# Optimization experiments

Measured on AMD Instinct MI355X. Metric: run time of the kernel, lower is better.

Reference implementation:

```python
import jax, jax.numpy as jnp
import numpy as np

B, W, H, I, L = 64, 4096, 128, 128, 2


def setup_inputs() -> dict:
    key = jax.random.key(0)
    ks = jax.random.split(key, 16)
    f = lambda k, s: jax.random.normal(k, s, dtype=jnp.float32) * 0.05
    return dict(
        input=f(ks[0], (B, 1, I)),
        h0=f(ks[1], (L, B, H)),
        c0=f(ks[2], (L, B, H)),
        encoder_output=f(ks[3], (B, W, H)),
        att_W=f(ks[4], (1, 2 * H)), att_b=f(ks[5], (1,)),
        inp_W=f(ks[6], (I, H + I)), inp_b=f(ks[7], (I,)),
        W_ih0=f(ks[8], (4 * H, I)), W_hh0=f(ks[9], (4 * H, H)),
        b_ih0=f(ks[10], (4 * H,)), b_hh0=f(ks[11], (4 * H,)),
        W_ih1=f(ks[12], (4 * H, H)), W_hh1=f(ks[13], (4 * H, H)),
        b_ih1=f(ks[14], (4 * H,)), b_hh1=f(ks[15], (4 * H,)),
    )


def _lstm_cell(x, h, c, W_ih, W_hh, b_ih, b_hh):
    # PyTorch gate order: i, f, g, o
    gates = x @ W_ih.T + h @ W_hh.T + b_ih + b_hh
    i, f, g, o = jnp.split(gates, 4, axis=-1)
    c_new = jax.nn.sigmoid(f) * c + jax.nn.sigmoid(i) * jnp.tanh(g)
    h_new = jax.nn.sigmoid(o) * jnp.tanh(c_new)
    return h_new, c_new


def reference(input, h0, c0, encoder_output, att_W, att_b, inp_W, inp_b,
              W_ih0, W_hh0, b_ih0, b_hh0, W_ih1, W_hh1, b_ih1, b_hh1):
    att_state = h0[-1] * c0[-1]                       # (B, H)
    # att_line over concat(enc_word, att_state): split the (1, 2H) weight.
    wa_enc, wa_st = att_W[0, :H], att_W[0, H:]
    scores = encoder_output @ wa_enc + (att_state @ wa_st + att_b[0])[:, None]  # (B, W)
    # Faithful to original: a leading zeros column is prepended, then
    # softmax is taken over [:, 0:-1] -> keeps the zero column, drops the
    # LAST word's score.
    zero_col = jnp.zeros((scores.shape[0], 1), scores.dtype)
    full = jnp.concatenate([zero_col, scores], axis=1)  # (B, W+1)
    weight = jax.nn.softmax(full[:, :-1], axis=1)        # (B, W)
    x = jnp.einsum('bw,bwh->bh', weight, encoder_output)  # (B, H)
    xin = jnp.concatenate([x, input[:, 0, :]], axis=1) @ inp_W.T + inp_b  # (B, I)
    # 2-layer LSTM, single time step (eval mode -> inter-layer dropout off)
    h1, c1 = _lstm_cell(xin, h0[0], c0[0], W_ih0, W_hh0, b_ih0, b_hh0)
    h2, c2 = _lstm_cell(h1, h0[1], c0[1], W_ih1, W_hh1, b_ih1, b_hh1)
    output = h2[:, None, :]                              # (B, 1, H)
    return output, jnp.stack([h1, h2]), jnp.stack([c1, c2])
```

## Files before the change

kernel.cpp:

```cpp
#include <hip/hip_runtime.h>
#include <hip/hip_bf16.h>

#define BB 64
#define WW 4096
#define HH 128

typedef unsigned short u16;
typedef unsigned int u32;

__device__ inline float bf2f(u16 u) {
    return __uint_as_float(((u32)u) << 16);
}
__device__ inline u16 f2bf(float f) {
    __hip_bfloat16 h = __float2bfloat16(f);
    return *reinterpret_cast<u16*>(&h);
}
__device__ inline void bf8_unpack(const uint4 r, float* o) {
    o[0] = __uint_as_float(r.x << 16);
    o[1] = __uint_as_float(r.x & 0xffff0000u);
    o[2] = __uint_as_float(r.y << 16);
    o[3] = __uint_as_float(r.y & 0xffff0000u);
    o[4] = __uint_as_float(r.z << 16);
    o[5] = __uint_as_float(r.z & 0xffff0000u);
    o[6] = __uint_as_float(r.w << 16);
    o[7] = __uint_as_float(r.w & 0xffff0000u);
}
__device__ inline float sigmoidf(float x) { return 1.0f / (1.0f + expf(-x)); }

template<bool FP32>
__device__ inline float ld1(const void* p, size_t i) {
    if (FP32) return ((const float*)p)[i];
    return bf2f(((const u16*)p)[i]);
}
template<bool FP32>
__device__ inline void ld8(const void* p, size_t g, float* o) {
    if (FP32) {
        float4 a = ((const float4*)p)[2 * g];
        float4 b = ((const float4*)p)[2 * g + 1];
        o[0] = a.x; o[1] = a.y; o[2] = a.z; o[3] = a.w;
        o[4] = b.x; o[5] = b.y; o[6] = b.z; o[7] = b.w;
    } else {
        uint4 r = ((const uint4*)p)[g];
        bf8_unpack(r, o);
    }
}
template<bool FP32>
__device__ inline void st1(void* p, size_t i, float v) {
    if (FP32) ((float*)p)[i] = v;
    else      ((u16*)p)[i] = f2bf(v);
}

__global__ void sniff_kernel(const u32* __restrict__ encw, float* __restrict__ flag) {
    __shared__ int red[256];
    const int t = threadIdx.x;
    u32 w = encw[(size_t)t * 997];
    float v = bf2f((u16)(w & 0xffffu));
    red[t] = (fabsf(v) <= 4.0f) ? 1 : 0;
    __syncthreads();
    for (int s = 128; s > 0; s >>= 1) {
        if (t < s) red[t] += red[t + s];
        __syncthreads();
    }
    if (t == 0) flag[0] = (red[0] >= 240) ? 1.0f : 0.0f;
}

template<bool FP32>
__global__ void scores_kernel(const void* __restrict__ enc,
                              const void* __restrict__ h0,
                              const void* __restrict__ c0,
                              const void* __restrict__ attW,
                              const void* __restrict__ attb,
                              const float* __restrict__ flag,
                              float* __restrict__ scores) {
    if ((flag[0] < 0.5f) != FP32) return;
    __shared__ float s_red[128];
    __shared__ float s_wa[128];
    __shared__ float s_bias;
    const int t = threadIdx.x;
    const int b = blockIdx.x >> 4;

    if (t < 128) {
        s_wa[t] = ld1<FP32>(attW, t);
        float hv = ld1<FP32>(h0, BB * HH + b * HH + t);
        float cv = ld1<FP32>(c0, BB * HH + b * HH + t);
        float ws = ld1<FP32>(attW, HH + t);
        s_red[t] = hv * cv * ws;
    }
    __syncthreads();
    for (int s = 64; s > 0; s >>= 1) {
        if (t < s) s_red[t] += s_red[t + s];
        __syncthreads();
    }
    if (t == 0) s_bias = s_red[0] + ld1<FP32>(attb, 0);
    __syncthreads();
    const float bias = s_bias;

    const int seg = t & 15;
    const int rg  = t >> 4;
    float wseg[8];
#pragma unroll
    for (int j = 0; j < 8; j++) wseg[j] = s_wa[seg * 8 + j];

    const size_t rowbase = (size_t)blockIdx.x * 256;
#pragma unroll 4
    for (int pass = 0; pass < 16; pass++) {
        const size_t row = rowbase + pass * 16 + rg;
        float v[8];
        ld8<FP32>(enc, row * 16 + seg, v);
        float d = 0.f;
#pragma unroll
        for (int j = 0; j < 8; j++) d += v[j] * wseg[j];
        d += __shfl_xor(d, 8, 16);
        d += __shfl_xor(d, 4, 16);
        d += __shfl_xor(d, 2, 16);
        d += __shfl_xor(d, 1, 16);
        if (seg == 0) scores[row] = d + bias;
    }
}

__global__ void softmax_kernel(const float* __restrict__ scores,
                               float* __restrict__ weight) {
    __shared__ float red[256];
    const int b = blockIdx.x;
    const int t = threadIdx.x;

    float lmax = -1e30f;
    for (int j = t; j < WW; j += 256) {
        float v = (j == 0) ? 0.f : scores[b * WW + j - 1];
        lmax = fmaxf(lmax, v);
    }
    red[t] = lmax;
    __syncthreads();
    for (int s = 128; s > 0; s >>= 1) {
        if (t < s) red[t] = fmaxf(red[t], red[t + s]);
        __syncthreads();
    }
    const float m = red[0];
    __syncthreads();

    float lsum = 0.f;
    for (int j = t; j < WW; j += 256) {
        float v = (j == 0) ? 0.f : scores[b * WW + j - 1];
        lsum += expf(v - m);
    }
    red[t] = lsum;
    __syncthreads();
    for (int s = 128; s > 0; s >>= 1) {
        if (t < s) red[t] += red[t + s];
        __syncthreads();
    }
    const float inv = 1.0f / red[0];
    __syncthreads();

    for (int j = t; j < WW; j += 256) {
        float v = (j == 0) ? 0.f : scores[b * WW + j - 1];
        weight[b * WW + j] = expf(v - m) * inv;
    }
}

__global__ void zero_x(float* __restrict__ x) {
    x[blockIdx.x * 1024 + threadIdx.x] = 0.f;
}

template<bool FP32>
__global__ void wsum_kernel(const void* __restrict__ enc,
                            const float* __restrict__ weight,
                            const float* __restrict__ flag,
                            float* __restrict__ x) {
    if ((flag[0] < 0.5f) != FP32) return;
    __shared__ float red[16 * 128];
    const int b = blockIdx.x >> 4;
    const int chunk = blockIdx.x & 15;
    const int t = threadIdx.x;
    const int seg = t & 15;
    const int wsub = t >> 4;

    float acc[8];
#pragma unroll
    for (int j = 0; j < 8; j++) acc[j] = 0.f;

    const int wbase = chunk * 256;
#pragma unroll 4
    for (int i = 0; i < 16; i++) {
        const int w = wbase + wsub + 16 * i;
        const float wt = weight[b * WW + w];
        float v[8];
        ld8<FP32>(enc, ((size_t)(b * WW + w)) * 16 + seg, v);
#pragma unroll
        for (int j = 0; j < 8; j++) acc[j] += wt * v[j];
    }
#pragma unroll
    for (int j = 0; j < 8; j++) red[wsub * 128 + seg * 8 + j] = acc[j];
    __syncthreads();
    if (t < 128) {
        float s = 0.f;
#pragma unroll
        for (int w2 = 0; w2 < 16; w2++) s += red[w2 * 128 + t];
        atomicAdd(&x[b * HH + t], s);
    }
}

template<bool FP32>
__global__ void xin_kernel(const float* __restrict__ x,
                           const void* __restrict__ input,
                           const void* __restrict__ inpW,
                           const void* __restrict__ inpb,
                           const float* __restrict__ flag,
                           float* __restrict__ xin) {
    if ((flag[0] < 0.5f) != FP32) return;
    __shared__ float xc[256];
    const int b = blockIdx.x;
    const int t = threadIdx.x;
    xc[t] = x[b * HH + t];
    xc[128 + t] = ld1<FP32>(input, b * HH + t);
    __syncthreads();
    float acc = ld1<FP32>(inpb, t);
#pragma unroll
    for (int k = 0; k < 256; k += 8) {
        float v[8];
        ld8<FP32>(inpW, ((size_t)t * 256 + k) >> 3, v);
#pragma unroll
        for (int j = 0; j < 8; j++) acc += xc[k + j] * v[j];
    }
    xin[b * HH + t] = acc;
}

template<bool FP32>
__global__ void lstm_kernel(const float* __restrict__ xv_in,
                            const void* __restrict__ hprev,
                            const void* __restrict__ cprev,
                            const void* __restrict__ W_ih,
                            const void* __restrict__ W_hh,
                            const void* __restrict__ b_ih,
                            const void* __restrict__ b_hh,
                            const float* __restrict__ flag,
                            float* __restrict__ hF_out,
                            void* __restrict__ h_out,
                            void* __restrict__ h_out2,
                            void* __restrict__ c_out) {
    if ((flag[0] < 0.5f) != FP32) return;
    __shared__ float xv[128];
    __shared__ float hv[128];
    __shared__ float gates[512];
    const int b = blockIdx.x;
    const int t = threadIdx.x;

    if (t < 128) {
        xv[t] = xv_in[b * HH + t];
        hv[t] = ld1<FP32>(hprev, b * HH + t);
    }
    __syncthreads();

    float acc = ld1<FP32>(b_ih, t) + ld1<FP32>(b_hh, t);
#pragma unroll
    for (int k = 0; k < 128; k += 8) {
        float v1[8], v2[8];
        ld8<FP32>(W_ih, ((size_t)t * 128 + k) >> 3, v1);
        ld8<FP32>(W_hh, ((size_t)t * 128 + k) >> 3, v2);
#pragma unroll
        for (int j = 0; j < 8; j++) acc += xv[k + j] * v1[j] + hv[k + j] * v2[j];
    }
    gates[t] = acc;
    __syncthreads();

    if (t < 128) {
        float ig = sigmoidf(gates[t]);
        float fg = sigmoidf(gates[128 + t]);
        float gg = tanhf(gates[256 + t]);
        float og = sigmoidf(gates[384 + t]);
        float cn = fg * ld1<FP32>(cprev, b * HH + t) + ig * gg;
        float hn = og * tanhf(cn);
        if (hF_out) hF_out[b * HH + t] = hn;
        st1<FP32>(h_out, b * HH + t, hn);
        if (h_out2) st1<FP32>(h_out2, b * HH + t, hn);
        st1<FP32>(c_out, b * HH + t, cn);
    }
}

extern "C" void kernel_launch(void* const* d_in, const int* in_sizes, int n_in,
                              void* d_out, int out_size, void* d_ws, size_t ws_size,
                              hipStream_t stream) {
    const void* input = d_in[0];
    const void* h0    = d_in[1];
    const void* c0    = d_in[2];
    const void* enc   = d_in[3];
    const void* attW  = d_in[4];
    const void* attb  = d_in[5];
    const void* inpW  = d_in[6];
    const void* inpb  = d_in[7];
    const void* Wih0  = d_in[8];
    const void* Whh0  = d_in[9];
    const void* bih0  = d_in[10];
    const void* bhh0  = d_in[11];
    const void* Wih1  = d_in[12];
    const void* Whh1  = d_in[13];
    const void* bih1  = d_in[14];
    const void* bhh1  = d_in[15];

    char* outc = (char*)d_out;

    float* wsf    = (float*)d_ws;
    float* scores = wsf;
    float* weight = wsf + (size_t)BB * WW;
    float* x      = weight + (size_t)BB * WW;
    float* xin    = x + BB * HH;
    float* h1f    = xin + BB * HH;
    float* flag   = h1f + BB * HH;

    sniff_kernel<<<1, 256, 0, stream>>>((const u32*)enc, flag);

    scores_kernel<false><<<BB * WW / 256, 256, 0, stream>>>(enc, h0, c0, attW, attb, flag, scores);
    scores_kernel<true ><<<BB * WW / 256, 256, 0, stream>>>(enc, h0, c0, attW, attb, flag, scores);
    softmax_kernel<<<BB, 256, 0, stream>>>(scores, weight);
    zero_x<<<8, 1024, 0, stream>>>(x);
    wsum_kernel<false><<<BB * 16, 256, 0, stream>>>(enc, weight, flag, x);
    wsum_kernel<true ><<<BB * 16, 256, 0, stream>>>(enc, weight, flag, x);
    xin_kernel<false><<<BB, 128, 0, stream>>>(x, input, inpW, inpb, flag, xin);
    xin_kernel<true ><<<BB, 128, 0, stream>>>(x, input, inpW, inpb, flag, xin);

    void* o_h1_b = outc + 8192 * 2;  void* o_h1_f = outc + 8192 * 4;
    void* o_h2_b = outc + 16384 * 2; void* o_h2_f = outc + 16384 * 4;
    void* o_c1_b = outc + 24576 * 2; void* o_c1_f = outc + 24576 * 4;
    void* o_c2_b = outc + 32768 * 2; void* o_c2_f = outc + 32768 * 4;

    lstm_kernel<false><<<BB, 512, 0, stream>>>(xin, h0, c0, Wih0, Whh0, bih0, bhh0, flag,
                                               h1f, o_h1_b, (void*)nullptr, o_c1_b);
    lstm_kernel<true ><<<BB, 512, 0, stream>>>(xin, h0, c0, Wih0, Whh0, bih0, bhh0, flag,
                                               h1f, o_h1_f, (void*)nullptr, o_c1_f);

    const char* h0l1_b = (const char*)h0 + BB * HH * 2;
    const char* c0l1_b = (const char*)c0 + BB * HH * 2;
    const char* h0l1_f = (const char*)h0 + BB * HH * 4;
    const char* c0l1_f = (const char*)c0 + BB * HH * 4;

    lstm_kernel<false><<<BB, 512, 0, stream>>>(h1f, h0l1_b, c0l1_b, Wih1, Whh1, bih1, bhh1, flag,
                                               (float*)nullptr, o_h2_b, d_out, o_c2_b);
    lstm_kernel<true ><<<BB, 512, 0, stream>>>(h1f, h0l1_f, c0l1_f, Wih1, Whh1, bih1, bhh1, flag,
                                               (float*)nullptr, o_h2_f, d_out, o_c2_f);
}
```

Baseline: 319.1 us.

## Fuse scores, softmax and weighted sum into one flash-style attention kernel

Replaces the sniff/scores/softmax/wsum/xin/lstm kernel chain with two kernels. The first computes chunk-local scores, an online softmax max and sum, and the weighted encoder sum in one pass, writing per-chunk partials. A tail kernel merges the partials and runs the input projection plus both LSTM layers. This drops the bf16/fp32 dual-launch path and the scores/weight round trips through global memory. The encoder is still read twice per chunk, the second time shifted by one row, though the second read may hit cache.

Result: faster. 285.6 us (-10.5%).

```diff
diff --git a/kernel.cpp b/kernel.cpp
--- a/kernel.cpp
+++ b/kernel.cpp
@@ -1,97 +1,43 @@
 #include <hip/hip_runtime.h>
-#include <hip/hip_bf16.h>
 
 #define BB 64
 #define WW 4096
 #define HH 128
-
-typedef unsigned short u16;
-typedef unsigned int u32;
-
-__device__ inline float bf2f(u16 u) {
-    return __uint_as_float(((u32)u) << 16);
-}
-__device__ inline u16 f2bf(float f) {
-    __hip_bfloat16 h = __float2bfloat16(f);
-    return *reinterpret_cast<u16*>(&h);
-}
-__device__ inline void bf8_unpack(const uint4 r, float* o) {
-    o[0] = __uint_as_float(r.x << 16);
-    o[1] = __uint_as_float(r.x & 0xffff0000u);
-    o[2] = __uint_as_float(r.y << 16);
-    o[3] = __uint_as_float(r.y & 0xffff0000u);
-    o[4] = __uint_as_float(r.z << 16);
-    o[5] = __uint_as_float(r.z & 0xffff0000u);
-    o[6] = __uint_as_float(r.w << 16);
-    o[7] = __uint_as_float(r.w & 0xffff0000u);
-}
+#define NCHUNK 32
+#define CROWS 128
+#define PSTRIDE 132
+
 __device__ inline float sigmoidf(float x) { return 1.0f / (1.0f + expf(-x)); }
 
-template<bool FP32>
-__device__ inline float ld1(const void* p, size_t i) {
-    if (FP32) return ((const float*)p)[i];
-    return bf2f(((const u16*)p)[i]);
-}
-template<bool FP32>
-__device__ inline void ld8(const void* p, size_t g, float* o) {
-    if (FP32) {
-        float4 a = ((const float4*)p)[2 * g];
-        float4 b = ((const float4*)p)[2 * g + 1];
-        o[0] = a.x; o[1] = a.y; o[2] = a.z; o[3] = a.w;
-        o[4] = b.x; o[5] = b.y; o[6] = b.z; o[7] = b.w;
-    } else {
-        uint4 r = ((const uint4*)p)[g];
-        bf8_unpack(r, o);
-    }
-}
-template<bool FP32>
-__device__ inline void st1(void* p, size_t i, float v) {
-    if (FP32) ((float*)p)[i] = v;
-    else      ((u16*)p)[i] = f2bf(v);
-}
-
-__global__ void sniff_kernel(const u32* __restrict__ encw, float* __restrict__ flag) {
-    __shared__ int red[256];
+__global__ void fused_attention(const float* __restrict__ enc,
+                                const float* __restrict__ h0,
+                                const float* __restrict__ c0,
+                                const float* __restrict__ attW,
+                                const float* __restrict__ attb,
+                                float* __restrict__ partials) {
+    __shared__ float s_wa[128];
+    __shared__ float s_red[128];
+    __shared__ float s_sc[CROWS];
+    __shared__ float racc[16 * 128];
+    __shared__ float s_bias, s_m, s_l;
+
     const int t = threadIdx.x;
-    u32 w = encw[(size_t)t * 997];
-    float v = bf2f((u16)(w & 0xffffu));
-    red[t] = (fabsf(v) <= 4.0f) ? 1 : 0;
-    __syncthreads();
-    for (int s = 128; s > 0; s >>= 1) {
-        if (t < s) red[t] += red[t + s];
-        __syncthreads();
-    }
-    if (t == 0) flag[0] = (red[0] >= 240) ? 1.0f : 0.0f;
-}
-
-template<bool FP32>
-__global__ void scores_kernel(const void* __restrict__ enc,
-                              const void* __restrict__ h0,
-                              const void* __restrict__ c0,
-                              const void* __restrict__ attW,
-                              const void* __restrict__ attb,
-                              const float* __restrict__ flag,
-                              float* __restrict__ scores) {
-    if ((flag[0] < 0.5f) != FP32) return;
-    __shared__ float s_red[128];
-    __shared__ float s_wa[128];
-    __shared__ float s_bias;
-    const int t = threadIdx.x;
-    const int b = blockIdx.x >> 4;
-
-    if (t < 128) {
-        s_wa[t] = ld1<FP32>(attW, t);
-        float hv = ld1<FP32>(h0, BB * HH + b * HH + t);
-        float cv = ld1<FP32>(c0, BB * HH + b * HH + t);
-        float ws = ld1<FP32>(attW, HH + t);
-        s_red[t] = hv * cv * ws;
+    const int b = blockIdx.x >> 5;
+    const int chunk = blockIdx.x & 31;
+    const int w0 = chunk * CROWS;
+
+    if (t < 128) {
+        s_wa[t] = attW[t];
+        float hv = h0[BB * HH + b * HH + t];
+        float cv = c0[BB * HH + b * HH + t];
+        s_red[t] = hv * cv * attW[HH + t];
     }
     __syncthreads();
     for (int s = 64; s > 0; s >>= 1) {
         if (t < s) s_red[t] += s_red[t + s];
         __syncthreads();
     }
-    if (t == 0) s_bias = s_red[0] + ld1<FP32>(attb, 0);
+    if (t == 0) s_bias = s_red[0] + attb[0];
     __syncthreads();
     const float bias = s_bias;
 
@@ -101,240 +47,223 @@
 #pragma unroll
     for (int j = 0; j < 8; j++) wseg[j] = s_wa[seg * 8 + j];
 
-    const size_t rowbase = (size_t)blockIdx.x * 256;
-#pragma unroll 4
-    for (int pass = 0; pass < 16; pass++) {
-        const size_t row = rowbase + pass * 16 + rg;
-        float v[8];
-        ld8<FP32>(enc, row * 16 + seg, v);
-        float d = 0.f;
-#pragma unroll
-        for (int j = 0; j < 8; j++) d += v[j] * wseg[j];
+#pragma unroll
+    for (int pass = 0; pass < 8; pass++) {
+        const int r = pass * 16 + rg;
+        const size_t w = (size_t)w0 + r;
+        const float4* p = (const float4*)(enc + ((size_t)b * WW + w) * HH + seg * 8);
+        float4 a = p[0], c = p[1];
+        float d = a.x * wseg[0] + a.y * wseg[1] + a.z * wseg[2] + a.w * wseg[3]
+                + c.x * wseg[4] + c.y * wseg[5] + c.z * wseg[6] + c.w * wseg[7];
         d += __shfl_xor(d, 8, 16);
         d += __shfl_xor(d, 4, 16);
         d += __shfl_xor(d, 2, 16);
         d += __shfl_xor(d, 1, 16);
-        if (seg == 0) scores[row] = d + bias;
-    }
+        if (seg == 0) s_sc[r] = (w == WW - 1) ? -1e30f : (d + bias);
+    }
+    __syncthreads();
+
+    if (t < 64) s_red[t] = fmaxf(s_sc[t], s_sc[t + 64]);
+    __syncthreads();
+    for (int s = 32; s > 0; s >>= 1) {
+        if (t < s) s_red[t] = fmaxf(s_red[t], s_red[t + s]);
+        __syncthreads();
+    }
+    if (t == 0) s_m = s_red[0];
+    __syncthreads();
+    const float m = s_m;
+
+    if (t < 128) s_sc[t] = expf(s_sc[t] - m);
+    __syncthreads();
+    if (t < 64) s_red[t] = s_sc[t] + s_sc[t + 64];
+    __syncthreads();
+    for (int s = 32; s > 0; s >>= 1) {
+        if (t < s) s_red[t] += s_red[t + s];
+        __syncthreads();
+    }
+    if (t == 0) s_l = s_red[0];
+
+    const int wsub = t >> 4;
+    float acc8[8];
+#pragma unroll
+    for (int j = 0; j < 8; j++) acc8[j] = 0.f;
+#pragma unroll
+    for (int pass = 0; pass < 8; pass++) {
+        const int r = pass * 16 + wsub;
+        const size_t w = (size_t)w0 + r;
+        if (w + 1 < WW) {
+            const float pw = s_sc[r];
+            const float4* p = (const float4*)(enc + ((size_t)b * WW + w + 1) * HH + seg * 8);
+            float4 a = p[0], c = p[1];
+            acc8[0] += pw * a.x; acc8[1] += pw * a.y;
+            acc8[2] += pw * a.z; acc8[3] += pw * a.w;
+            acc8[4] += pw * c.x; acc8[5] += pw * c.y;
+            acc8[6] += pw * c.z; acc8[7] += pw * c.w;
+        }
+    }
+#pragma unroll
+    for (int j = 0; j < 8; j++) racc[wsub * 128 + seg * 8 + j] = acc8[j];
+    __syncthreads();
+
+    float* out = partials + (size_t)(b * NCHUNK + chunk) * PSTRIDE;
+    if (t < 128) {
+        float s = 0.f;
+#pragma unroll
+        for (int w2 = 0; w2 < 16; w2++) s += racc[w2 * 128 + t];
+        out[t] = s;
+    }
+    if (t == 128) out[128] = m;
+    if (t == 129) out[129] = s_l;
 }
 
-__global__ void softmax_kernel(const float* __restrict__ scores,
-                               float* __restrict__ weight) {
-    __shared__ float red[256];
+__global__ void tail_kernel(const float* __restrict__ partials,
+                            const float* __restrict__ enc,
+                            const float* __restrict__ input,
+                            const float* __restrict__ inpW,
+                            const float* __restrict__ inpb,
+                            const float* __restrict__ Wih0,
+                            const float* __restrict__ Whh0,
+                            const float* __restrict__ bih0,
+                            const float* __restrict__ bhh0,
+                            const float* __restrict__ Wih1,
+                            const float* __restrict__ Whh1,
+                            const float* __restrict__ bih1,
+                            const float* __restrict__ bhh1,
+                            const float* __restrict__ h0,
+                            const float* __restrict__ c0,
+                            float* __restrict__ out) {
+    __shared__ float lm[NCHUNK], llv[NCHUNK], ls[NCHUNK];
+    __shared__ float sM, sL;
+    __shared__ float xc[256];
+    __shared__ float sxv[128];
+    __shared__ float shv[128];
+    __shared__ float sh1[128];
+    __shared__ float shv2[128];
+    __shared__ float gates[512];
+
     const int b = blockIdx.x;
     const int t = threadIdx.x;
 
-    float lmax = -1e30f;
-    for (int j = t; j < WW; j += 256) {
-        float v = (j == 0) ? 0.f : scores[b * WW + j - 1];
-        lmax = fmaxf(lmax, v);
-    }
-    red[t] = lmax;
-    __syncthreads();
-    for (int s = 128; s > 0; s >>= 1) {
-        if (t < s) red[t] = fmaxf(red[t], red[t + s]);
-        __syncthreads();
-    }
-    const float m = red[0];
-    __syncthreads();
-
-    float lsum = 0.f;
-    for (int j = t; j < WW; j += 256) {
-        float v = (j == 0) ? 0.f : scores[b * WW + j - 1];
-        lsum += expf(v - m);
-    }
-    red[t] = lsum;
-    __syncthreads();
-    for (int s = 128; s > 0; s >>= 1) {
-        if (t < s) red[t] += red[t + s];
-        __syncthreads();
-    }
-    const float inv = 1.0f / red[0];
-    __syncthreads();
-
-    for (int j = t; j < WW; j += 256) {
-        float v = (j == 0) ? 0.f : scores[b * WW + j - 1];
-        weight[b * WW + j] = expf(v - m) * inv;
-    }
-}
-
-__global__ void zero_x(float* __restrict__ x) {
-    x[blockIdx.x * 1024 + threadIdx.x] = 0.f;
-}
-
-template<bool FP32>
-__global__ void wsum_kernel(const void* __restrict__ enc,
-                            const float* __restrict__ weight,
-                            const float* __restrict__ flag,
-                            float* __restrict__ x) {
-    if ((flag[0] < 0.5f) != FP32) return;
-    __shared__ float red[16 * 128];
-    const int b = blockIdx.x >> 4;
-    const int chunk = blockIdx.x & 15;
-    const int t = threadIdx.x;
-    const int seg = t & 15;
-    const int wsub = t >> 4;
-
-    float acc[8];
-#pragma unroll
-    for (int j = 0; j < 8; j++) acc[j] = 0.f;
-
-    const int wbase = chunk * 256;
-#pragma unroll 4
-    for (int i = 0; i < 16; i++) {
-        const int w = wbase + wsub + 16 * i;
-        const float wt = weight[b * WW + w];
-        float v[8];
-        ld8<FP32>(enc, ((size_t)(b * WW + w)) * 16 + seg, v);
-#pragma unroll
-        for (int j = 0; j < 8; j++) acc[j] += wt * v[j];
-    }
-#pragma unroll
-    for (int j = 0; j < 8; j++) red[wsub * 128 + seg * 8 + j] = acc[j];
-    __syncthreads();
-    if (t < 128) {
-        float s = 0.f;
-#pragma unroll
-        for (int w2 = 0; w2 < 16; w2++) s += red[w2 * 128 + t];
-        atomicAdd(&x[b * HH + t], s);
-    }
-}
-
-template<bool FP32>
-__global__ void xin_kernel(const float* __restrict__ x,
-                           const void* __restrict__ input,
-                           const void* __restrict__ inpW,
-                           const void* __restrict__ inpb,
-                           const float* __restrict__ flag,
-                           float* __restrict__ xin) {
-    if ((flag[0] < 0.5f) != FP32) return;
-    __shared__ float xc[256];
-    const int b = blockIdx.x;
-    const int t = threadIdx.x;
-    xc[t] = x[b * HH + t];
-    xc[128 + t] = ld1<FP32>(input, b * HH + t);
-    __syncthreads();
-    float acc = ld1<FP32>(inpb, t);
-#pragma unroll
-    for (int k = 0; k < 256; k += 8) {
-        float v[8];
-        ld8<FP32>(inpW, ((size_t)t * 256 + k) >> 3, v);
-#pragma unroll
-        for (int j = 0; j < 8; j++) acc += xc[k + j] * v[j];
-    }
-    xin[b * HH + t] = acc;
-}
-
-template<bool FP32>
-__global__ void lstm_kernel(const float* __restrict__ xv_in,
-                            const void* __restrict__ hprev,
-                            const void* __restrict__ cprev,
-                            const void* __restrict__ W_ih,
-                            const void* __restrict__ W_hh,
-                            const void* __restrict__ b_ih,
-                            const void* __restrict__ b_hh,
-                            const float* __restrict__ flag,
-                            float* __restrict__ hF_out,
-                            void* __restrict__ h_out,
-                            void* __restrict__ h_out2,
-                            void* __restrict__ c_out) {
-    if ((flag[0] < 0.5f) != FP32) return;
-    __shared__ float xv[128];
-    __shared__ float hv[128];
-    __shared__ float gates[512];
-    const int b = blockIdx.x;
-    const int t = threadIdx.x;
-
-    if (t < 128) {
-        xv[t] = xv_in[b * HH + t];
-        hv[t] = ld1<FP32>(hprev, b * HH + t);
-    }
-    __syncthreads();
-
-    float acc = ld1<FP32>(b_ih, t) + ld1<FP32>(b_hh, t);
-#pragma unroll
-    for (int k = 0; k < 128; k += 8) {
-        float v1[8], v2[8];
-        ld8<FP32>(W_ih, ((size_t)t * 128 + k) >> 3, v1);
-        ld8<FP32>(W_hh, ((size_t)t * 128 + k) >> 3, v2);
-#pragma unroll
-        for (int j = 0; j < 8; j++) acc += xv[k + j] * v1[j] + hv[k + j] * v2[j];
-    }
-    gates[t] = acc;
-    __syncthreads();
-
+    if (t < NCHUNK) {
+        const float* pp = partials + (size_t)(b * NCHUNK + t) * PSTRIDE;
+        lm[t] = pp[128];
+        llv[t] = pp[129];
+    }
+    __syncthreads();
+    if (t == 0) {
+        float M = 0.0f;
+        for (int c = 0; c < NCHUNK; c++) M = fmaxf(M, lm[c]);
+        float L = expf(-M);
+        for (int c = 0; c < NCHUNK; c++) {
+            float s = expf(lm[c] - M);
+            ls[c] = s;
+            L += s * llv[c];
+        }
+        sM = M; sL = L;
+    }
+    __syncthreads();
+
+    if (t < 128) {
+        float xv = expf(-sM) * enc[(size_t)b * WW * HH + t];
+        for (int c = 0; c < NCHUNK; c++)
+            xv += ls[c] * partials[(size_t)(b * NCHUNK + c) * PSTRIDE + t];
+        xc[t] = xv / sL;
+        xc[128 + t] = input[b * HH + t];
+    }
+    __syncthreads();
+
+    if (t < 128) {
+        float a = inpb[t];
+        const float4* wr = (const float4*)(inpW + (size_t)t * 256);
+#pragma unroll
+        for (int k = 0; k < 64; k++) {
+            float4 w4 = wr[k];
+            a += xc[4 * k] * w4.x + xc[4 * k + 1] * w4.y
+               + xc[4 * k + 2] * w4.z + xc[4 * k + 3] * w4.w;
+        }
+        sxv[t] = a;
+        shv[t] = h0[b * HH + t];
+        shv2[t] = h0[BB * HH + b * HH + t];
+    }
+    __syncthreads();
+
+    {
+        float g = bih0[t] + bhh0[t];
+        const float4* wi = (const float4*)(Wih0 + (size_t)t * 128);
+        const float4* wh = (const float4*)(Whh0 + (size_t)t * 128);
+#pragma unroll
+        for (int k = 0; k < 32; k++) {
+            float4 a = wi[k], c = wh[k];
+            g += sxv[4 * k] * a.x + sxv[4 * k + 1] * a.y + sxv[4 * k + 2] * a.z + sxv[4 * k + 3] * a.w
+               + shv[4 * k] * c.x + shv[4 * k + 1] * c.y + shv[4 * k + 2] * c.z + shv[4 * k + 3] * c.w;
+        }
+        gates[t] = g;
+    }
+    __syncthreads();
     if (t < 128) {
         float ig = sigmoidf(gates[t]);
         float fg = sigmoidf(gates[128 + t]);
         float gg = tanhf(gates[256 + t]);
         float og = sigmoidf(gates[384 + t]);
-        float cn = fg * ld1<FP32>(cprev, b * HH + t) + ig * gg;
+        float cn = fg * c0[b * HH + t] + ig * gg;
         float hn = og * tanhf(cn);
-        if (hF_out) hF_out[b * HH + t] = hn;
-        st1<FP32>(h_out, b * HH + t, hn);
-        if (h_out2) st1<FP32>(h_out2, b * HH + t, hn);
-        st1<FP32>(c_out, b * HH + t, cn);
+        out[8192 + b * HH + t] = hn;
+        out[24576 + b * HH + t] = cn;
+        sh1[t] = hn;
+    }
+    __syncthreads();
+
+    {
+        float g = bih1[t] + bhh1[t];
+        const float4* wi = (const float4*)(Wih1 + (size_t)t * 128);
+        const float4* wh = (const float4*)(Whh1 + (size_t)t * 128);
+#pragma unroll
+        for (int k = 0; k < 32; k++) {
+            float4 a = wi[k], c = wh[k];
+            g += sh1[4 * k] * a.x + sh1[4 * k + 1] * a.y + sh1[4 * k + 2] * a.z + sh1[4 * k + 3] * a.w
+               + shv2[4 * k] * c.x + shv2[4 * k + 1] * c.y + shv2[4 * k + 2] * c.z + shv2[4 * k + 3] * c.w;
+        }
+        gates[t] = g;
+    }
+    __syncthreads();
+    if (t < 128) {
+        float ig = sigmoidf(gates[t]);
+        float fg = sigmoidf(gates[128 + t]);
+        float gg = tanhf(gates[256 + t]);
+        float og = sigmoidf(gates[384 + t]);
+        float cn = fg * c0[BB * HH + b * HH + t] + ig * gg;
+        float hn = og * tanhf(cn);
+        out[b * HH + t] = hn;
+        out[16384 + b * HH + t] = hn;
+        out[32768 + b * HH + t] = cn;
     }
 }
 
 extern "C" void kernel_launch(void* const* d_in, const int* in_sizes, int n_in,
                               void* d_out, int out_size, void* d_ws, size_t ws_size,
                               hipStream_t stream) {
-    const void* input = d_in[0];
-    const void* h0    = d_in[1];
-    const void* c0    = d_in[2];
-    const void* enc   = d_in[3];
-    const void* attW  = d_in[4];
-    const void* attb  = d_in[5];
-    const void* inpW  = d_in[6];
-    const void* inpb  = d_in[7];
-    const void* Wih0  = d_in[8];
-    const void* Whh0  = d_in[9];
-    const void* bih0  = d_in[10];
-    const void* bhh0  = d_in[11];
-    const void* Wih1  = d_in[12];
-    const void* Whh1  = d_in[13];
-    const void* bih1  = d_in[14];
-    const void* bhh1  = d_in[15];
-
-    char* outc = (char*)d_out;
-
-    float* wsf    = (float*)d_ws;
-    float* scores = wsf;
-    float* weight = wsf + (size_t)BB * WW;
-    float* x      = weight + (size_t)BB * WW;
-    float* xin    = x + BB * HH;
-    float* h1f    = xin + BB * HH;
-    float* flag   = h1f + BB * HH;
-
-    sniff_kernel<<<1, 256, 0, stream>>>((const u32*)enc, flag);
-
-    scores_kernel<false><<<BB * WW / 256, 256, 0, stream>>>(enc, h0, c0, attW, attb, flag, scores);
-    scores_kernel<true ><<<BB * WW / 256, 256, 0, stream>>>(enc, h0, c0, attW, attb, flag, scores);
-    softmax_kernel<<<BB, 256, 0, stream>>>(scores, weight);
-    zero_x<<<8, 1024, 0, stream>>>(x);
-    wsum_kernel<false><<<BB * 16, 256, 0, stream>>>(enc, weight, flag, x);
-    wsum_kernel<true ><<<BB * 16, 256, 0, stream>>>(enc, weight, flag, x);
-    xin_kernel<false><<<BB, 128, 0, stream>>>(x, input, inpW, inpb, flag, xin);
-    xin_kernel<true ><<<BB, 128, 0, stream>>>(x, input, inpW, inpb, flag, xin);
-
-    void* o_h1_b = outc + 8192 * 2;  void* o_h1_f = outc + 8192 * 4;
-    void* o_h2_b = outc + 16384 * 2; void* o_h2_f = outc + 16384 * 4;
-    void* o_c1_b = outc + 24576 * 2; void* o_c1_f = outc + 24576 * 4;
-    void* o_c2_b = outc + 32768 * 2; void* o_c2_f = outc + 32768 * 4;
-
-    lstm_kernel<false><<<BB, 512, 0, stream>>>(xin, h0, c0, Wih0, Whh0, bih0, bhh0, flag,
-                                               h1f, o_h1_b, (void*)nullptr, o_c1_b);
-    lstm_kernel<true ><<<BB, 512, 0, stream>>>(xin, h0, c0, Wih0, Whh0, bih0, bhh0, flag,
-                                               h1f, o_h1_f, (void*)nullptr, o_c1_f);
-
-    const char* h0l1_b = (const char*)h0 + BB * HH * 2;
-    const char* c0l1_b = (const char*)c0 + BB * HH * 2;
-    const char* h0l1_f = (const char*)h0 + BB * HH * 4;
-    const char* c0l1_f = (const char*)c0 + BB * HH * 4;
-
-    lstm_kernel<false><<<BB, 512, 0, stream>>>(h1f, h0l1_b, c0l1_b, Wih1, Whh1, bih1, bhh1, flag,
-                                               (float*)nullptr, o_h2_b, d_out, o_c2_b);
-    lstm_kernel<true ><<<BB, 512, 0, stream>>>(h1f, h0l1_f, c0l1_f, Wih1, Whh1, bih1, bhh1, flag,
-                                               (float*)nullptr, o_h2_f, d_out, o_c2_f);
+    const float* input = (const float*)d_in[0];
+    const float* h0    = (const float*)d_in[1];
+    const float* c0    = (const float*)d_in[2];
+    const float* enc   = (const float*)d_in[3];
+    const float* attW  = (const float*)d_in[4];
+    const float* attb  = (const float*)d_in[5];
+    const float* inpW  = (const float*)d_in[6];
+    const float* inpb  = (const float*)d_in[7];
+    const float* Wih0  = (const float*)d_in[8];
+    const float* Whh0  = (const float*)d_in[9];
+    const float* bih0  = (const float*)d_in[10];
+    const float* bhh0  = (const float*)d_in[11];
+    const float* Wih1  = (const float*)d_in[12];
+    const float* Whh1  = (const float*)d_in[13];
+    const float* bih1  = (const float*)d_in[14];
+    const float* bhh1  = (const float*)d_in[15];
+
+    float* partials = (float*)d_ws;
+
+    fused_attention<<<BB * NCHUNK, 256, 0, stream>>>(enc, h0, c0, attW, attb, partials);
+    tail_kernel<<<BB, 512, 0, stream>>>(partials, enc, input, inpW, inpb,
+                                        Wih0, Whh0, bih0, bhh0,
+                                        Wih1, Whh1, bih1, bhh1,
+                                        h0, c0, (float*)d_out);
 }
```
